# Kernel optimization log

Measured on AMD Instinct MI355X. Metric: run time of the kernel, lower is better.

The kernel has to match this reference:

```python
import jax, jax.numpy as jnp
import numpy as np


def fwht(x):
    """Fast Walsh-Hadamard transform over the last dim (power of 2), normalized by 1/sqrt(n)."""
    n = x.shape[-1]
    orig_shape = x.shape
    x = x.reshape(-1, n)
    h = 1
    while h < n:
        x = x.reshape(-1, n // (2 * h), 2, h)
        a = x[:, :, 0, :]
        b = x[:, :, 1, :]
        x = jnp.stack([a + b, a - b], axis=2)
        h *= 2
    x = x.reshape(orig_shape)
    return x * (1.0 / jnp.sqrt(jnp.asarray(n, dtype=x.dtype)))


def act_quant(x, bits):
    """Per-token absmax symmetric quantization with straight-through estimator."""
    qb = 2.0 ** (bits - 1) - 1.0  # 127 for 8 bits
    scale = qb / jnp.clip(jnp.max(jnp.abs(x), axis=-1, keepdims=True), 1e-5, None)
    q = jnp.clip(jnp.round(x * scale), -qb, qb) / scale
    return x + jax.lax.stop_gradient(q - x)


def weight_quant(w):
    """BitNet b1.58 ternary weight quantization (per-tensor mean-abs scale) with STE."""
    scale = jnp.clip(jnp.mean(jnp.abs(w)), 1e-5, None)
    q = jnp.clip(jnp.round(w / scale), -1.0, 1.0) * scale
    return w + jax.lax.stop_gradient(q - w)


def hbitlinear(x, w, bits):
    # Hadamard rotate activations, quantize acts + ternary weights, then GEMM.
    xh = fwht(x)
    xq = act_quant(xh, bits)
    wq = weight_quant(w)
    return jnp.einsum('bsh,oh->bso', xq, wq)


def setup_inputs() -> dict:
    key = jax.random.key(0)
    k1, k2, k3 = jax.random.split(key, 3)
    B, S, H = 4, 2048, 2048
    I = 4096  # intermediate = hidden * mlp_ratio(2.0)
    hidden_states = jax.random.normal(k1, (B, S, H), dtype=jnp.float32)
    w_up = jax.random.normal(k2, (I, H), dtype=jnp.float32) * 0.02
    w_down = jax.random.normal(k3, (H, I), dtype=jnp.float32) * 0.02
    return {"hidden_states": hidden_states, "w_up": w_up, "w_down": w_down}


def reference(hidden_states, w_up, w_down):
    ACT_BITS = 8
    h = hbitlinear(hidden_states, w_up, ACT_BITS)   # (B, S, I)
    h = jnp.square(jax.nn.relu(h))                  # ReLU^2
    # dropout with p=0.0 (eval/identity)
    out = hbitlinear(h, w_down, ACT_BITS)           # (B, S, H)
    return out
```

## Files before the change

kernel.cpp:

```cpp
#include <hip/hip_runtime.h>
#include <hip/hip_bf16.h>

typedef int i32x4 __attribute__((ext_vector_type(4)));

#define GLL16(g, l) __builtin_amdgcn_global_load_lds( \
    (const __attribute__((address_space(1))) void*)(g), \
    (__attribute__((address_space(3))) void*)(l), 16, 0, 0)

#define CFENCE() asm volatile("" ::: "memory")

__global__ __launch_bounds__(256) void abs_sum_kernel(const float* __restrict__ w, int n4,
                                                      double* __restrict__ out)
{
    double acc = 0.0;
    const float4* w4 = (const float4*)w;
    for (int i = blockIdx.x * blockDim.x + threadIdx.x; i < n4; i += gridDim.x * blockDim.x) {
        float4 v = w4[i];
        acc += (double)fabsf(v.x) + (double)fabsf(v.y) + (double)fabsf(v.z) + (double)fabsf(v.w);
    }
    for (int o = 32; o > 0; o >>= 1) acc += __shfl_down(acc, o, 64);
    __shared__ double part[4];
    int lane = threadIdx.x & 63, wv = threadIdx.x >> 6;
    if (lane == 0) part[wv] = acc;
    __syncthreads();
    if (threadIdx.x == 0) atomicAdd(out, part[0] + part[1] + part[2] + part[3]);
}

__global__ __launch_bounds__(256) void wquant_kernel(const float* __restrict__ w, int n4,
                                                     const double* __restrict__ sum, double inv_count,
                                                     char* __restrict__ out)
{
    float s = (float)(sum[0] * inv_count);
    s = fmaxf(s, 1e-5f);
    const float4* w4 = (const float4*)w;
    char4* o4 = (char4*)out;
    for (int i = blockIdx.x * blockDim.x + threadIdx.x; i < n4; i += gridDim.x * blockDim.x) {
        float4 v = w4[i];
        char4 c;
        c.x = (char)fminf(fmaxf(rintf(v.x / s), -1.0f), 1.0f);
        c.y = (char)fminf(fmaxf(rintf(v.y / s), -1.0f), 1.0f);
        c.z = (char)fminf(fmaxf(rintf(v.z / s), -1.0f), 1.0f);
        c.w = (char)fminf(fmaxf(rintf(v.w / s), -1.0f), 1.0f);
        o4[i] = c;
    }
}

template<int NS>
__device__ __forceinline__ void hreg(float* v)
{
    #pragma unroll
    for (int h = 1; h < (1 << NS); h <<= 1)
        #pragma unroll
        for (int i = 0; i < 16; i++)
            if ((i & h) == 0) { float a = v[i], b = v[i + h]; v[i] = a + b; v[i + h] = a - b; }
}

template<int N, int TOKS>
__global__ __launch_bounds__(256) void fwht_quant_kernel(
    const float* __restrict__ in, long in_stride,
    char* __restrict__ outq, long out_stride,
    float* __restrict__ scales)
{
    constexpr int L = 256 / TOKS;
    static_assert(N == 16 * L, "N must be 16*threads-per-token");
    __shared__ float sx[TOKS * N];
    __shared__ float red[4];

    const int tid = threadIdx.x;
    const int tk  = tid / L;
    const int lt  = tid % L;
    const long tok = (long)blockIdx.x * TOKS + tk;
    const float* row = in + tok * in_stride;
    float* s = sx + tk * N;

    float v[16];
    {
        const float4* r4 = (const float4*)(row + (size_t)lt * 16);
        float4 a[4];
        #pragma unroll
        for (int i = 0; i < 4; i++) a[i] = r4[i];
        #pragma unroll
        for (int i = 0; i < 4; i++) {
            v[4*i] = a[i].x; v[4*i+1] = a[i].y; v[4*i+2] = a[i].z; v[4*i+3] = a[i].w;
        }
    }
    hreg<4>(v);
    #pragma unroll
    for (int i = 0; i < 4; i++)
        *(float4*)(s + lt * 16 + 4 * i) = make_float4(v[4*i], v[4*i+1], v[4*i+2], v[4*i+3]);
    __syncthreads();

    const int o = lt & 15, ss = lt >> 4;
    #pragma unroll
    for (int j = 0; j < 16; j++) v[j] = s[o + 256 * ss + 16 * j];
    hreg<(L == 256) ? 4 : 3>(v);
    #pragma unroll
    for (int j = 0; j < 16; j++) s[o + 256 * ss + 16 * j] = v[j];
    __syncthreads();

    #pragma unroll
    for (int j = 0; j < 16; j++) v[j] = s[o + 16 * ss + L * j];
    hreg<4>(v);

    const float rn = 1.0f / sqrtf((float)N);
    float m = 0.0f;
    #pragma unroll
    for (int j = 0; j < 16; j++) { v[j] *= rn; m = fmaxf(m, fabsf(v[j])); }
    for (int off = 32; off > 0; off >>= 1) m = fmaxf(m, __shfl_down(m, off, 64));
    if ((tid & 63) == 0) red[tid >> 6] = m;
    __syncthreads();
    float mm;
    if (TOKS == 1) mm = fmaxf(fmaxf(red[0], red[1]), fmaxf(red[2], red[3]));
    else           mm = fmaxf(red[2 * tk], red[2 * tk + 1]);
    mm = fmaxf(mm, 1e-5f);
    const float sc = 127.0f / mm;
    if (lt == 0) scales[tok] = sc;
    __syncthreads();

    char* ct = (char*)sx + tk * N;
    #pragma unroll
    for (int j = 0; j < 16; j++) {
        float q = fminf(fmaxf(rintf(v[j] * sc), -127.0f), 127.0f);
        ct[o + 16 * ss + L * j] = (char)q;
    }
    __syncthreads();
    int4* dst = (int4*)(outq + tok * out_stride);
    dst[lt] = ((const int4*)ct)[lt];
}

#define BM2 256
#define BN2 256
#define BK2 64

__global__ __launch_bounds__(512, 2) void gemm_bt_kernel(
    const char* __restrict__ A, int lda,
    const char* __restrict__ B, int ldb,
    float* __restrict__ C, int ldc,
    int K, int lognx,
    const float* __restrict__ sx,
    const double* __restrict__ wsum, double inv_count,
    int do_relu2)
{
    __shared__ __align__(16) char As[4][BM2 * BK2];
    __shared__ __align__(16) char Bs[4][BN2 * BK2];

    const int bid = blockIdx.x;
    const int xcd = bid & 7;
    const int n = bid >> 3;
    const int nper = gridDim.x >> 3;
    const int bx = n & ((1 << lognx) - 1);
    const int by = xcd * (nper >> lognx) + (n >> lognx);
    const int row0 = by * BM2;
    const int col0 = bx * BN2;

    const int tid = threadIdx.x;
    const int lane = tid & 63;
    const int w = tid >> 6;
    const int wr = w >> 2;
    const int wc = w & 3;

    i32x4 acc[8][4] = {};

    const int srow = w * 16 + (lane >> 2);
    const int sseg = ((lane & 3) ^ ((lane >> 3) & 3)) << 4;
    const char* Ag0 = A + (size_t)(row0 + srow) * lda + sseg;
    const char* Ag1 = Ag0 + (size_t)128 * lda;
    const char* Bg0 = B + (size_t)(col0 + srow) * ldb + sseg;
    const char* Bg1 = Bg0 + (size_t)128 * ldb;
    const int wdst = w * 1024;

    const int fr = lane & 15;
    const int fks = lane >> 4;
    const int rsw = ((fks ^ ((fr >> 1) & 3)) << 4);
    const int aoff = (wr * 128 + fr) * BK2 + rsw;
    const int boff = (wc * 64  + fr) * BK2 + rsw;

    const int NT = K >> 6;

    auto stageA = [&](int tt) {
        const int sb = tt & 3;
        const int ko = tt * BK2;
        GLL16(Ag0 + ko, &As[sb][wdst]);
        GLL16(Ag1 + ko, &As[sb][wdst + 8192]);
    };
    auto stageB = [&](int tt) {
        const int sb = tt & 3;
        const int ko = tt * BK2;
        GLL16(Bg0 + ko, &Bs[sb][wdst]);
        GLL16(Bg1 + ko, &Bs[sb][wdst + 8192]);
    };

    auto tile_body = [&](int t, bool do_stage) __attribute__((always_inline)) {
        const int cb = t & 3;
        const char* as = As[cb];
        const char* bs = Bs[cb];
        i32x4 af[4], bf[4], af2[4];
        #pragma unroll
        for (int i = 0; i < 4; ++i) af[i] = *(const i32x4*)(as + aoff + i * 1024);
        #pragma unroll
        for (int j = 0; j < 4; ++j) bf[j] = *(const i32x4*)(bs + boff + j * 1024);
        if (do_stage) stageA(t + 3);
        __builtin_amdgcn_s_barrier();
        CFENCE();
        __builtin_amdgcn_s_setprio(1);
        #pragma unroll
        for (int i = 0; i < 4; ++i)
            #pragma unroll
            for (int j = 0; j < 4; ++j)
                acc[i][j] = __builtin_amdgcn_mfma_i32_16x16x64_i8(af[i], bf[j], acc[i][j], 0, 0, 0);
        __builtin_amdgcn_s_setprio(0);
        __builtin_amdgcn_s_barrier();
        CFENCE();
        #pragma unroll
        for (int i = 0; i < 4; ++i) af2[i] = *(const i32x4*)(as + aoff + (4 + i) * 1024);
        if (do_stage) stageB(t + 3);
        __builtin_amdgcn_s_barrier();
        CFENCE();
        __builtin_amdgcn_s_setprio(1);
        #pragma unroll
        for (int i = 0; i < 4; ++i)
            #pragma unroll
            for (int j = 0; j < 4; ++j)
                acc[4 + i][j] = __builtin_amdgcn_mfma_i32_16x16x64_i8(af2[i], bf[j], acc[4 + i][j], 0, 0, 0);
        __builtin_amdgcn_s_setprio(0);
    };

    stageA(0); stageB(0); stageA(1); stageB(1); stageA(2); stageB(2);
    asm volatile("s_waitcnt vmcnt(8)" ::: "memory");
    __builtin_amdgcn_s_barrier();
    CFENCE();

    for (int t = 0; t <= NT - 4; ++t) {
        tile_body(t, true);
        asm volatile("s_waitcnt vmcnt(8)" ::: "memory");
        __builtin_amdgcn_s_barrier();
        CFENCE();
    }
    tile_body(NT - 3, false);
    asm volatile("s_waitcnt vmcnt(4)" ::: "memory");
    __builtin_amdgcn_s_barrier();
    CFENCE();
    tile_body(NT - 2, false);
    asm volatile("s_waitcnt vmcnt(0)" ::: "memory");
    __builtin_amdgcn_s_barrier();
    CFENCE();
    tile_body(NT - 1, false);

    float sw = (float)(wsum[0] * inv_count);
    sw = fmaxf(sw, 1e-5f);
    const int qd = lane >> 4;
    #pragma unroll
    for (int i = 0; i < 8; ++i) {
        #pragma unroll
        for (int r = 0; r < 4; ++r) {
            int rowm = row0 + wr * 128 + i * 16 + qd * 4 + r;
            float esc = sw / sx[rowm];
            float* crow = C + (size_t)rowm * ldc + col0 + wc * 64;
            #pragma unroll
            for (int j = 0; j < 4; ++j) {
                float v = (float)acc[i][j][r] * esc;
                if (do_relu2) { v = fmaxf(v, 0.0f); v = v * v; }
                crow[j * 16 + fr] = v;
            }
        }
    }
}

extern "C" void kernel_launch(void* const* d_in, const int* in_sizes, int n_in,
                              void* d_out, int out_size, void* d_ws, size_t ws_size,
                              hipStream_t stream)
{
    const float* X   = (const float*)d_in[0];
    const float* Wup = (const float*)d_in[1];
    const float* Wdn = (const float*)d_in[2];
    float* out = (float*)d_out;

    const int Mtok = 8192, H = 2048, I = 4096;
    const int NW = H * I;

    char* ws = (char*)d_ws;
    double* sums = (double*)ws;
    float* sx1 = (float*)(ws + 1024);
    float* sx2 = (float*)(ws + 1024 + 32768);
    char* wqup = ws + (1 << 20);
    char* wqdn = wqup + (size_t)NW;
    char* xq1  = wqdn + (size_t)NW;
    float* hbuf = (float*)(xq1 + (size_t)Mtok * H);

    hipMemsetAsync(sums, 0, 16, stream);
    abs_sum_kernel<<<512, 256, 0, stream>>>(Wup, NW / 4, &sums[0]);
    abs_sum_kernel<<<512, 256, 0, stream>>>(Wdn, NW / 4, &sums[1]);
    const double invc = 1.0 / (double)NW;
    wquant_kernel<<<1024, 256, 0, stream>>>(Wup, NW / 4, &sums[0], invc, wqup);
    wquant_kernel<<<1024, 256, 0, stream>>>(Wdn, NW / 4, &sums[1], invc, wqdn);

    fwht_quant_kernel<2048, 2><<<Mtok / 2, 256, 0, stream>>>(X, H, xq1, H, sx1);
    gemm_bt_kernel<<<(I / BN2) * (Mtok / BM2), 512, 0, stream>>>(
        xq1, H, wqup, H, hbuf, I, H, 4, sx1, &sums[0], invc, 1);
    fwht_quant_kernel<4096, 1><<<Mtok, 256, 0, stream>>>(hbuf, I, (char*)hbuf, 4 * I, sx2);
    gemm_bt_kernel<<<(H / BN2) * (Mtok / BM2), 512, 0, stream>>>(
        (const char*)hbuf, 4 * I, wqdn, I, out, H, I, 3, sx2, &sums[1], invc, 0);
}
```

Before: 399.8 us.

## Store intermediate activations in fp16, swizzle FWHT LDS, merge weight-prep kernels

```diff
diff --git a/kernel.cpp b/kernel.cpp
--- a/kernel.cpp
+++ b/kernel.cpp
@@ -1,5 +1,6 @@
 #include <hip/hip_runtime.h>
 #include <hip/hip_bf16.h>
+#include <hip/hip_fp16.h>
 
 typedef int i32x4 __attribute__((ext_vector_type(4)));
 
@@ -9,12 +10,15 @@
 
 #define CFENCE() asm volatile("" ::: "memory")
 
-__global__ __launch_bounds__(256) void abs_sum_kernel(const float* __restrict__ w, int n4,
-                                                      double* __restrict__ out)
-{
+__global__ __launch_bounds__(256) void abs_sum2_kernel(const float* __restrict__ w0,
+                                                       const float* __restrict__ w1, int n4,
+                                                       double* __restrict__ out)
+{
+    const int sel = blockIdx.x & 1;
+    const float4* w4 = (const float4*)(sel ? w1 : w0);
+    const int b = blockIdx.x >> 1, nb = gridDim.x >> 1;
     double acc = 0.0;
-    const float4* w4 = (const float4*)w;
-    for (int i = blockIdx.x * blockDim.x + threadIdx.x; i < n4; i += gridDim.x * blockDim.x) {
+    for (int i = b * blockDim.x + threadIdx.x; i < n4; i += nb * blockDim.x) {
         float4 v = w4[i];
         acc += (double)fabsf(v.x) + (double)fabsf(v.y) + (double)fabsf(v.z) + (double)fabsf(v.w);
     }
@@ -23,18 +27,21 @@
     int lane = threadIdx.x & 63, wv = threadIdx.x >> 6;
     if (lane == 0) part[wv] = acc;
     __syncthreads();
-    if (threadIdx.x == 0) atomicAdd(out, part[0] + part[1] + part[2] + part[3]);
-}
-
-__global__ __launch_bounds__(256) void wquant_kernel(const float* __restrict__ w, int n4,
-                                                     const double* __restrict__ sum, double inv_count,
-                                                     char* __restrict__ out)
-{
-    float s = (float)(sum[0] * inv_count);
+    if (threadIdx.x == 0) atomicAdd(&out[sel], part[0] + part[1] + part[2] + part[3]);
+}
+
+__global__ __launch_bounds__(256) void wquant2_kernel(const float* __restrict__ w0,
+                                                      const float* __restrict__ w1, int n4,
+                                                      const double* __restrict__ sums, double inv_count,
+                                                      char* __restrict__ o0, char* __restrict__ o1)
+{
+    const int sel = blockIdx.x & 1;
+    const float4* w4 = (const float4*)(sel ? w1 : w0);
+    char4* o4 = (char4*)(sel ? o1 : o0);
+    float s = (float)(sums[sel] * inv_count);
     s = fmaxf(s, 1e-5f);
-    const float4* w4 = (const float4*)w;
-    char4* o4 = (char4*)out;
-    for (int i = blockIdx.x * blockDim.x + threadIdx.x; i < n4; i += gridDim.x * blockDim.x) {
+    const int b = blockIdx.x >> 1, nb = gridDim.x >> 1;
+    for (int i = b * blockDim.x + threadIdx.x; i < n4; i += nb * blockDim.x) {
         float4 v = w4[i];
         char4 c;
         c.x = (char)fminf(fmaxf(rintf(v.x / s), -1.0f), 1.0f);
@@ -55,6 +62,12 @@
             if ((i & h) == 0) { float a = v[i], b = v[i + h]; v[i] = a + b; v[i + h] = a - b; }
 }
 
+__device__ __forceinline__ int lswz(int e)
+{
+    const int r16 = e >> 4;
+    return r16 * 16 + 4 * (((e >> 2) & 3) ^ ((r16 >> 1) & 3)) + (e & 3);
+}
+
 template<int N, int TOKS>
 __global__ __launch_bounds__(256) void fwht_quant_kernel(
     const float* __restrict__ in, long in_stride,
@@ -85,21 +98,25 @@
         }
     }
     hreg<4>(v);
-    #pragma unroll
-    for (int i = 0; i < 4; i++)
-        *(float4*)(s + lt * 16 + 4 * i) = make_float4(v[4*i], v[4*i+1], v[4*i+2], v[4*i+3]);
+    {
+        const int psw = (lt >> 1) & 3;
+        #pragma unroll
+        for (int i = 0; i < 4; i++)
+            *(float4*)(s + lt * 16 + 4 * (i ^ psw)) =
+                make_float4(v[4*i], v[4*i+1], v[4*i+2], v[4*i+3]);
+    }
     __syncthreads();
 
     const int o = lt & 15, ss = lt >> 4;
     #pragma unroll
-    for (int j = 0; j < 16; j++) v[j] = s[o + 256 * ss + 16 * j];
+    for (int j = 0; j < 16; j++) v[j] = s[lswz(o + 256 * ss + 16 * j)];
     hreg<(L == 256) ? 4 : 3>(v);
     #pragma unroll
-    for (int j = 0; j < 16; j++) s[o + 256 * ss + 16 * j] = v[j];
-    __syncthreads();
-
-    #pragma unroll
-    for (int j = 0; j < 16; j++) v[j] = s[o + 16 * ss + L * j];
+    for (int j = 0; j < 16; j++) s[lswz(o + 256 * ss + 16 * j)] = v[j];
+    __syncthreads();
+
+    #pragma unroll
+    for (int j = 0; j < 16; j++) v[j] = s[lswz(o + 16 * ss + L * j)];
     hreg<4>(v);
 
     const float rn = 1.0f / sqrtf((float)N);
@@ -128,6 +145,83 @@
     dst[lt] = ((const int4*)ct)[lt];
 }
 
+__global__ __launch_bounds__(256) void fwht_quant_f16_kernel(
+    const __half* __restrict__ in, long in_stride,
+    char* __restrict__ outq, long out_stride,
+    float* __restrict__ scales)
+{
+    constexpr int N = 4096, L = 256;
+    __shared__ float sx[N];
+    __shared__ float red[4];
+
+    const int lt = threadIdx.x;
+    const long tok = blockIdx.x;
+    const __half* row = in + tok * in_stride;
+    float* s = sx;
+
+    float v[16];
+    {
+        const int4* r4 = (const int4*)row;
+        int4 q0 = r4[2 * lt], q1 = r4[2 * lt + 1];
+        const __half2* h0 = (const __half2*)&q0;
+        const __half2* h1 = (const __half2*)&q1;
+        #pragma unroll
+        for (int i = 0; i < 4; i++) {
+            float2 f = __half22float2(h0[i]);
+            v[2*i] = f.x; v[2*i+1] = f.y;
+        }
+        #pragma unroll
+        for (int i = 0; i < 4; i++) {
+            float2 f = __half22float2(h1[i]);
+            v[8+2*i] = f.x; v[8+2*i+1] = f.y;
+        }
+    }
+    hreg<4>(v);
+    {
+        const int psw = (lt >> 1) & 3;
+        #pragma unroll
+        for (int i = 0; i < 4; i++)
+            *(float4*)(s + lt * 16 + 4 * (i ^ psw)) =
+                make_float4(v[4*i], v[4*i+1], v[4*i+2], v[4*i+3]);
+    }
+    __syncthreads();
+
+    const int o = lt & 15, ss = lt >> 4;
+    #pragma unroll
+    for (int j = 0; j < 16; j++) v[j] = s[lswz(o + 256 * ss + 16 * j)];
+    hreg<4>(v);
+    #pragma unroll
+    for (int j = 0; j < 16; j++) s[lswz(o + 256 * ss + 16 * j)] = v[j];
+    __syncthreads();
+
+    #pragma unroll
+    for (int j = 0; j < 16; j++) v[j] = s[lswz(o + 16 * ss + L * j)];
+    hreg<4>(v);
+
+    const float rn = 1.0f / sqrtf((float)N);
+    float m = 0.0f;
+    #pragma unroll
+    for (int j = 0; j < 16; j++) { v[j] *= rn; m = fmaxf(m, fabsf(v[j])); }
+    for (int off = 32; off > 0; off >>= 1) m = fmaxf(m, __shfl_down(m, off, 64));
+    if ((lt & 63) == 0) red[lt >> 6] = m;
+    __syncthreads();
+    float mm = fmaxf(fmaxf(red[0], red[1]), fmaxf(red[2], red[3]));
+    mm = fmaxf(mm, 1e-5f);
+    const float sc = 127.0f / mm;
+    if (lt == 0) scales[tok] = sc;
+    __syncthreads();
+
+    char* ct = (char*)sx;
+    #pragma unroll
+    for (int j = 0; j < 16; j++) {
+        float q = fminf(fmaxf(rintf(v[j] * sc), -127.0f), 127.0f);
+        ct[o + 16 * ss + L * j] = (char)q;
+    }
+    __syncthreads();
+    int4* dst = (int4*)(outq + tok * out_stride);
+    dst[lt] = ((const int4*)ct)[lt];
+}
+
 #define BM2 256
 #define BN2 256
 #define BK2 64
@@ -135,11 +229,11 @@
 __global__ __launch_bounds__(512, 2) void gemm_bt_kernel(
     const char* __restrict__ A, int lda,
     const char* __restrict__ B, int ldb,
-    float* __restrict__ C, int ldc,
+    void* __restrict__ Cv, int ldc,
     int K, int lognx,
     const float* __restrict__ sx,
     const double* __restrict__ wsum, double inv_count,
-    int do_relu2)
+    int do_relu2, int out_f16)
 {
     __shared__ __align__(16) char As[4][BM2 * BK2];
     __shared__ __align__(16) char Bs[4][BN2 * BK2];
@@ -249,18 +343,38 @@
     float sw = (float)(wsum[0] * inv_count);
     sw = fmaxf(sw, 1e-5f);
     const int qd = lane >> 4;
-    #pragma unroll
-    for (int i = 0; i < 8; ++i) {
-        #pragma unroll
-        for (int r = 0; r < 4; ++r) {
-            int rowm = row0 + wr * 128 + i * 16 + qd * 4 + r;
-            float esc = sw / sx[rowm];
-            float* crow = C + (size_t)rowm * ldc + col0 + wc * 64;
+    if (out_f16) {
+        __half* C = (__half*)Cv;
+        #pragma unroll
+        for (int i = 0; i < 8; ++i) {
             #pragma unroll
-            for (int j = 0; j < 4; ++j) {
-                float v = (float)acc[i][j][r] * esc;
-                if (do_relu2) { v = fmaxf(v, 0.0f); v = v * v; }
-                crow[j * 16 + fr] = v;
+            for (int r = 0; r < 4; ++r) {
+                int rowm = row0 + wr * 128 + i * 16 + qd * 4 + r;
+                float esc = sw / sx[rowm];
+                __half* crow = C + (size_t)rowm * ldc + col0 + wc * 64;
+                #pragma unroll
+                for (int j = 0; j < 4; ++j) {
+                    float v = (float)acc[i][j][r] * esc;
+                    if (do_relu2) { v = fmaxf(v, 0.0f); v = v * v; }
+                    crow[j * 16 + fr] = __float2half(v);
+                }
+            }
+        }
+    } else {
+        float* C = (float*)Cv;
+        #pragma unroll
+        for (int i = 0; i < 8; ++i) {
+            #pragma unroll
+            for (int r = 0; r < 4; ++r) {
+                int rowm = row0 + wr * 128 + i * 16 + qd * 4 + r;
+                float esc = sw / sx[rowm];
+                float* crow = C + (size_t)rowm * ldc + col0 + wc * 64;
+                #pragma unroll
+                for (int j = 0; j < 4; ++j) {
+                    float v = (float)acc[i][j][r] * esc;
+                    if (do_relu2) { v = fmaxf(v, 0.0f); v = v * v; }
+                    crow[j * 16 + fr] = v;
+                }
             }
         }
     }
@@ -285,19 +399,17 @@
     char* wqup = ws + (1 << 20);
     char* wqdn = wqup + (size_t)NW;
     char* xq1  = wqdn + (size_t)NW;
-    float* hbuf = (float*)(xq1 + (size_t)Mtok * H);
+    char* hbuf = xq1 + (size_t)Mtok * H;
 
     hipMemsetAsync(sums, 0, 16, stream);
-    abs_sum_kernel<<<512, 256, 0, stream>>>(Wup, NW / 4, &sums[0]);
-    abs_sum_kernel<<<512, 256, 0, stream>>>(Wdn, NW / 4, &sums[1]);
+    abs_sum2_kernel<<<1024, 256, 0, stream>>>(Wup, Wdn, NW / 4, sums);
     const double invc = 1.0 / (double)NW;
-    wquant_kernel<<<1024, 256, 0, stream>>>(Wup, NW / 4, &sums[0], invc, wqup);
-    wquant_kernel<<<1024, 256, 0, stream>>>(Wdn, NW / 4, &sums[1], invc, wqdn);
+    wquant2_kernel<<<2048, 256, 0, stream>>>(Wup, Wdn, NW / 4, sums, invc, wqup, wqdn);
 
     fwht_quant_kernel<2048, 2><<<Mtok / 2, 256, 0, stream>>>(X, H, xq1, H, sx1);
     gemm_bt_kernel<<<(I / BN2) * (Mtok / BM2), 512, 0, stream>>>(
-        xq1, H, wqup, H, hbuf, I, H, 4, sx1, &sums[0], invc, 1);
-    fwht_quant_kernel<4096, 1><<<Mtok, 256, 0, stream>>>(hbuf, I, (char*)hbuf, 4 * I, sx2);
+        xq1, H, wqup, H, hbuf, I, H, 4, sx1, &sums[0], invc, 1, 1);
+    fwht_quant_f16_kernel<<<Mtok, 256, 0, stream>>>((const __half*)hbuf, I, hbuf, 2 * I, sx2);
     gemm_bt_kernel<<<(H / BN2) * (Mtok / BM2), 512, 0, stream>>>(
-        (const char*)hbuf, 4 * I, wqdn, I, out, H, I, 3, sx2, &sums[1], invc, 0);
-}
+        (const char*)hbuf, 2 * I, wqdn, I, out, H, I, 3, sx2, &sums[1], invc, 0, 0);
+}
```

After: 372.3 us. -6.9%, faster.
